# Performance work log

Measured on AMD Instinct MI355X. Metric: run time of the kernel, lower is better.

## Reference

```python
import jax, jax.numpy as jnp
import numpy as np

N_NODES = 50000
N_EDGES = 800000
IN_CH = 128
CH = 128
OUT_CH = 128
N_TAPS = 3
N_LAYERS = 2


def setup_inputs() -> dict:
    key = jax.random.key(0)
    ks = jax.random.split(key, 8)
    s = 0.05
    x = jax.random.normal(ks[0], (N_NODES, IN_CH), dtype=jnp.float32)
    edge_index = jax.random.randint(ks[1], (2, N_EDGES), 0, N_NODES)
    # readin MLP: 1 layer, plain_last=False -> Linear + activation
    w_in = jax.random.normal(ks[2], (IN_CH, CH), dtype=jnp.float32) * s
    b_in = jnp.zeros((CH,), jnp.float32)
    # per-layer GraphFilter taps: (n_taps+1) Linears of [CH, CH]
    taps_w = jax.random.normal(ks[3], (N_LAYERS, N_TAPS + 1, CH, CH), dtype=jnp.float32) * s
    taps_b = jax.random.normal(ks[4], (N_LAYERS, N_TAPS + 1, CH), dtype=jnp.float32) * s
    # readout MLP: 1 layer, plain_last=True -> Linear only
    w_out = jax.random.normal(ks[5], (CH, OUT_CH), dtype=jnp.float32) * s
    b_out = jnp.zeros((OUT_CH,), jnp.float32)
    return {
        "x": x,
        "edge_index": edge_index,
        "w_in": w_in,
        "b_in": b_in,
        "taps_w": taps_w,
        "taps_b": taps_b,
        "w_out": w_out,
        "b_out": b_out,
    }


def reference(x, edge_index, w_in, b_in, taps_w, taps_b, w_out, b_out):
    act = jax.nn.leaky_relu  # torch LeakyReLU default negative_slope=0.01
    src, dst = edge_index[0], edge_index[1]
    n = x.shape[0]

    # readin: Linear + act (plain_last=False)
    h = act(x @ w_in + b_in)

    n_layers, n_taps_p1 = taps_w.shape[0], taps_w.shape[1]
    for l in range(n_layers):
        # ResidualBlock: y = act(h); y = GraphFilter(y); h = h + y
        y = act(h)
        out = y @ taps_w[l, 0] + taps_b[l, 0]
        for k in range(1, n_taps_p1):
            # SimpleConv(aggr='sum'): y_i = sum_{(s->i) in E} y_s
            y = jax.ops.segment_sum(y[src], dst, num_segments=n)
            out = out + y @ taps_w[l, k] + taps_b[l, k]
        h = h + out

    # readout: Linear only (plain_last=True)
    return h @ w_out + b_out
```

## Files before the change

kernel.cpp:

```cpp
#include <hip/hip_runtime.h>

typedef unsigned int uint;
typedef unsigned short ushort;

using bf16x8 = __attribute__((ext_vector_type(8))) short;
using f32x4  = __attribute__((ext_vector_type(4))) float;

__device__ __forceinline__ float lrelu(float v) { return v > 0.f ? v : 0.01f * v; }
__device__ __forceinline__ float b2f(ushort u) { return __uint_as_float((uint)u << 16); }
__device__ __forceinline__ ushort f2b(float f) {
  uint u = __float_as_uint(f);
  u += 0x7fffu + ((u >> 16) & 1u);
  return (ushort)(u >> 16);
}

#define CSR_B 256
#define BKT_SHIFT 10
#define MAX_NB 64


template <int MODE, int K>
__global__ __launch_bounds__(256) void gemm_mfma(
    const ushort* __restrict__ A0, const ushort* __restrict__ A1,
    const ushort* __restrict__ A2, const ushort* __restrict__ A3,
    const ushort* __restrict__ Wt, const float* __restrict__ bias,
    float* __restrict__ h, ushort* __restrict__ yout, int do_act, int N) {
  __shared__ ushort As[64][40];
  __shared__ ushort Bs[128][40];
  const int tid = threadIdx.x;
  const int lane = tid & 63;
  const int wave = tid >> 6;
  const int g = lane >> 4;
  const int mr = lane & 15;
  const int wr = wave >> 1;
  const int wc = wave & 1;
  const int row0 = blockIdx.x * 64;

  const ushort* Ap[4] = {A0, A1, A2, A3};

  f32x4 acc[2][4];
#pragma unroll
  for (int i = 0; i < 2; i++)
#pragma unroll
    for (int j = 0; j < 4; j++) acc[i][j] = (f32x4){0.f, 0.f, 0.f, 0.f};

#pragma unroll 4
  for (int kc = 0; kc < K; kc += 32) {
    {
      int m = tid >> 2, q = tid & 3;
      int r = row0 + m;
      if (r >= N) r = N - 1;
      int kg = kc + q * 8;
      const ushort* ap = Ap[kg >> 7] + ((size_t)((kg >> 5) & 3)) * N * 32 +
                         (size_t)r * 32 + (kg & 31);
      *(uint4*)&As[m][q * 8] = *(const uint4*)ap;
    }
#pragma unroll
    for (int t = 0; t < 2; t++) {
      int slot = tid + t * 256;
      int n = slot >> 2, q = slot & 3;
      *(uint4*)&Bs[n][q * 8] = *(const uint4*)(Wt + (size_t)n * K + kc + q * 8);
    }
    __syncthreads();
    bf16x8 af[2], bf[4];
#pragma unroll
    for (int rt = 0; rt < 2; rt++) af[rt] = *(bf16x8*)&As[wr * 32 + rt * 16 + mr][g * 8];
#pragma unroll
    for (int ct = 0; ct < 4; ct++) bf[ct] = *(bf16x8*)&Bs[wc * 64 + ct * 16 + mr][g * 8];
#pragma unroll
    for (int rt = 0; rt < 2; rt++)
#pragma unroll
      for (int ct = 0; ct < 4; ct++)
        acc[rt][ct] = __builtin_amdgcn_mfma_f32_16x16x32_bf16(af[rt], bf[ct], acc[rt][ct], 0, 0, 0);
    __syncthreads();
  }

#pragma unroll
  for (int rt = 0; rt < 2; rt++) {
#pragma unroll
    for (int i = 0; i < 4; i++) {
      int R = row0 + wr * 32 + rt * 16 + g * 4 + i;
      if (R >= N) continue;
#pragma unroll
      for (int ct = 0; ct < 4; ct++) {
        int c = wc * 64 + ct * 16 + mr;
        float v = acc[rt][ct][i] + bias[c];
        size_t o = (size_t)R * 128 + c;
        size_t oy = (size_t)(c >> 5) * N * 32 + (size_t)R * 32 + (c & 31);
        if (MODE == 0) {
          float hv = lrelu(v);
          h[o] = hv;
          yout[oy] = f2b(lrelu(hv));
        } else if (MODE == 1) {
          float hv = h[o] + v;
          h[o] = hv;
          if (yout) yout[oy] = f2b(do_act ? lrelu(hv) : hv);
        } else {
          h[o] = v;
        }
      }
    }
  }
}

__global__ __launch_bounds__(256) void agg_bf16(const ushort* __restrict__ yin,
                                                ushort* __restrict__ yout,
                                                const int* __restrict__ rowp,
                                                const ushort* __restrict__ esrc, int N) {
  int t = threadIdx.x;
  int chunk = blockIdx.x & 3;
  int node = (blockIdx.x >> 2) * 64 + (t >> 2);
  if (node >= N) return;
  int lane = t & 3;
  const ushort* yb = yin + (size_t)chunk * N * 32 + lane * 8;
  int beg = rowp[node], end = rowp[node + 1];
  float s[8] = {0.f, 0.f, 0.f, 0.f, 0.f, 0.f, 0.f, 0.f};
  int j = beg;
  for (; j + 4 <= end; j += 4) {
    int s0 = esrc[j], s1 = esrc[j + 1], s2 = esrc[j + 2], s3 = esrc[j + 3];
    union { uint4 v; ushort u[8]; } w0, w1, w2, w3;
    w0.v = *(const uint4*)(yb + (size_t)s0 * 32);
    w1.v = *(const uint4*)(yb + (size_t)s1 * 32);
    w2.v = *(const uint4*)(yb + (size_t)s2 * 32);
    w3.v = *(const uint4*)(yb + (size_t)s3 * 32);
#pragma unroll
    for (int e = 0; e < 8; e++)
      s[e] += (b2f(w0.u[e]) + b2f(w1.u[e])) + (b2f(w2.u[e]) + b2f(w3.u[e]));
  }
  for (; j < end; j++) {
    int sn = esrc[j];
    union { uint4 v; ushort u[8]; } w;
    w.v = *(const uint4*)(yb + (size_t)sn * 32);
#pragma unroll
    for (int e = 0; e < 8; e++) s[e] += b2f(w.u[e]);
  }
  union { uint4 v; ushort u[8]; } o;
#pragma unroll
  for (int e = 0; e < 8; e++) o.u[e] = f2b(s[e]);
  *(uint4*)(yout + (size_t)chunk * N * 32 + (size_t)node * 32 + lane * 8) = o.v;
}

__global__ __launch_bounds__(256) void cast_f2b(const float* __restrict__ in,
                                                ushort* __restrict__ out, int N) {
  int i = blockIdx.x * 256 + threadIdx.x;
  if (i >= N * 16) return;
  int node = i >> 4, sub = i & 15;
  float4 a = *(const float4*)(in + (size_t)node * 128 + sub * 8);
  float4 b = *(const float4*)(in + (size_t)node * 128 + sub * 8 + 4);
  float v[8] = {a.x, a.y, a.z, a.w, b.x, b.y, b.z, b.w};
  union { uint4 q; ushort u[8]; } o;
#pragma unroll
  for (int e = 0; e < 8; e++) o.u[e] = f2b(v[e]);
  int chunk = sub >> 2, off = (sub & 3) * 8;
  *(uint4*)(out + (size_t)chunk * N * 32 + (size_t)node * 32 + off) = o.q;
}

__global__ __launch_bounds__(256) void prep_k(const float* __restrict__ w_in,
                                              const float* __restrict__ w_out,
                                              const float* __restrict__ taps_w,
                                              const float* __restrict__ taps_b,
                                              ushort* __restrict__ Wt_in,
                                              ushort* __restrict__ Wt_out,
                                              ushort* __restrict__ Wt_l0,
                                              ushort* __restrict__ Wt_l1,
                                              float* __restrict__ bsum) {
  int gid = blockIdx.x * 256 + threadIdx.x;
  if (gid < 16384) {
    int n = gid >> 7, k = gid & 127;
    Wt_in[gid] = f2b(w_in[k * 128 + n]);
  } else if (gid < 32768) {
    int i = gid - 16384;
    int n = i >> 7, k = i & 127;
    Wt_out[i] = f2b(w_out[k * 128 + n]);
  } else if (gid < 98304) {
    int i = gid - 32768;
    int n = i >> 9, k = i & 511;
    Wt_l0[i] = f2b(taps_w[(size_t)k * 128 + n]);
  } else if (gid < 163840) {
    int i = gid - 98304;
    int n = i >> 9, k = i & 511;
    Wt_l1[i] = f2b(taps_w[(size_t)(512 + k) * 128 + n]);
  } else if (gid < 164096) {
    int i = gid - 163840;
    int l = i >> 7, n = i & 127;
    float s = 0.f;
    for (int k = 0; k < 4; k++) s += taps_b[l * 512 + k * 128 + n];
    bsum[i] = s;
  }
}

__global__ __launch_bounds__(256) void chist_k(const int* __restrict__ dst,
                                               int* __restrict__ H, int E, int NB) {
  __shared__ int hh[MAX_NB];
  if (threadIdx.x < NB) hh[threadIdx.x] = 0;
  __syncthreads();
  int chunk = (E + gridDim.x - 1) / gridDim.x;
  int beg = blockIdx.x * chunk, end = min(E, beg + chunk);
  for (int e = beg + threadIdx.x; e < end; e += 256)
    atomicAdd(&hh[dst[e] >> BKT_SHIFT], 1);
  __syncthreads();
  if (threadIdx.x < NB) H[threadIdx.x * gridDim.x + blockIdx.x] = hh[threadIdx.x];
}

__global__ __launch_bounds__(256) void cscan_k(int* __restrict__ H, int M) {
  __shared__ int sm[256];
  int per = (M + 255) / 256;
  int b0 = threadIdx.x * per;
  int hi = min(M, b0 + per);
  int sum = 0;
  for (int i = b0; i < hi; i++) sum += H[i];
  sm[threadIdx.x] = sum;
  __syncthreads();
  int x = sum;
  for (int off = 1; off < 256; off <<= 1) {
    int tt = (threadIdx.x >= off) ? sm[threadIdx.x - off] : 0;
    __syncthreads();
    x += tt;
    sm[threadIdx.x] = x;
    __syncthreads();
  }
  int run = x - sum;
  for (int i = b0; i < hi; i++) {
    int v = H[i];
    H[i] = run;
    run += v;
  }
}

__global__ __launch_bounds__(256) void cscatter_k(const int* __restrict__ src,
                                                  const int* __restrict__ dst,
                                                  const int* __restrict__ H,
                                                  uint* __restrict__ packed,
                                                  int E, int NB) {
  __shared__ int cur[MAX_NB];
  int chunk = (E + gridDim.x - 1) / gridDim.x;
  int beg = blockIdx.x * chunk, end = min(E, beg + chunk);
  if (threadIdx.x < NB) cur[threadIdx.x] = H[threadIdx.x * gridDim.x + blockIdx.x];
  __syncthreads();
  for (int e = beg + threadIdx.x; e < end; e += 256) {
    int d = dst[e];
    int pos = atomicAdd(&cur[d >> BKT_SHIFT], 1);
    packed[pos] = ((uint)d << 16) | (uint)src[e];
  }
}

__global__ __launch_bounds__(256) void fsort_k(const uint* __restrict__ packed,
                                               const int* __restrict__ H,
                                               ushort* __restrict__ esrc,
                                               int* __restrict__ rowp,
                                               int N, int E, int NB) {
  __shared__ int hist[1 << BKT_SHIFT];
  __shared__ int cur[1 << BKT_SHIFT];
  __shared__ int sm[256];
  const int bkt = blockIdx.x;
  const int base = bkt << BKT_SHIFT;
  const int nb_nodes = min(1 << BKT_SHIFT, N - base);
  const int start = H[bkt * CSR_B];
  const int end = (bkt == NB - 1) ? E : H[(bkt + 1) * CSR_B];

  for (int i = threadIdx.x; i < (1 << BKT_SHIFT); i += 256) hist[i] = 0;
  __syncthreads();
  for (int e = start + threadIdx.x; e < end; e += 256)
    atomicAdd(&hist[(packed[e] >> 16) - base], 1);
  __syncthreads();

  int t4 = threadIdx.x * 4;
  int l0 = hist[t4], l1 = hist[t4 + 1], l2 = hist[t4 + 2], l3 = hist[t4 + 3];
  int ssum = l0 + l1 + l2 + l3;
  sm[threadIdx.x] = ssum;
  __syncthreads();
  int x = ssum;
  for (int off = 1; off < 256; off <<= 1) {
    int tt = (threadIdx.x >= off) ? sm[threadIdx.x - off] : 0;
    __syncthreads();
    x += tt;
    sm[threadIdx.x] = x;
    __syncthreads();
  }
  int c0 = start + x - ssum;
  int c1 = c0 + l0, c2 = c1 + l1, c3 = c2 + l2;
  cur[t4] = c0; cur[t4 + 1] = c1; cur[t4 + 2] = c2; cur[t4 + 3] = c3;
  if (t4 + 0 < nb_nodes) rowp[base + t4 + 0] = c0;
  if (t4 + 1 < nb_nodes) rowp[base + t4 + 1] = c1;
  if (t4 + 2 < nb_nodes) rowp[base + t4 + 2] = c2;
  if (t4 + 3 < nb_nodes) rowp[base + t4 + 3] = c3;
  __syncthreads();

  for (int e = start + threadIdx.x; e < end; e += 256) {
    uint p = packed[e];
    int pos = atomicAdd(&cur[(p >> 16) - base], 1);
    esrc[pos] = (ushort)(p & 0xffffu);
  }
  if (bkt == 0 && threadIdx.x == 0) rowp[N] = E;
}

extern "C" void kernel_launch(void* const* d_in, const int* in_sizes, int n_in,
                              void* d_out, int out_size, void* d_ws, size_t ws_size,
                              hipStream_t stream) {
  const float* x      = (const float*)d_in[0];
  const int*   ei     = (const int*)d_in[1];
  const float* w_in   = (const float*)d_in[2];
  const float* b_in   = (const float*)d_in[3];
  const float* taps_w = (const float*)d_in[4];
  const float* taps_b = (const float*)d_in[5];
  const float* w_out  = (const float*)d_in[6];
  const float* b_out  = (const float*)d_in[7];

  const int N = in_sizes[0] / 128;
  const int E = in_sizes[1] / 2;
  const int* src = ei;
  const int* dst = ei + E;
  const int NB = (N + (1 << BKT_SHIFT) - 1) >> BKT_SHIFT;

  float* h = (float*)d_out;

  const size_t yelem = (size_t)N * 128;
  ushort* y0 = (ushort*)d_ws;
  ushort* y1 = y0 + yelem;
  ushort* y2 = y1 + yelem;
  ushort* y3 = y2 + yelem;
  ushort* Wt_in  = y3 + yelem;
  ushort* Wt_out = Wt_in + 128 * 128;
  ushort* Wt_l0  = Wt_out + 128 * 128;
  ushort* Wt_l1  = Wt_l0 + 128 * 512;
  float*  bsum   = (float*)(Wt_l1 + 128 * 512);
  int*    rowp   = (int*)(bsum + 256);
  int*    H      = rowp + (N + 1);
  uint*   packed = (uint*)(H + MAX_NB * CSR_B);
  ushort* esrc   = (ushort*)(packed + E);

  const int gemmB = (N + 63) / 64;
  const int aggB  = ((N + 63) / 64) * 4;
  const int castB = (N * 16 + 255) / 256;

  chist_k<<<CSR_B, 256, 0, stream>>>(dst, H, E, NB);
  cscan_k<<<1, 256, 0, stream>>>(H, NB * CSR_B);
  cscatter_k<<<CSR_B, 256, 0, stream>>>(src, dst, H, packed, E, NB);
  fsort_k<<<NB, 256, 0, stream>>>(packed, H, esrc, rowp, N, E, NB);

  prep_k<<<641, 256, 0, stream>>>(w_in, w_out, taps_w, taps_b,
                                  Wt_in, Wt_out, Wt_l0, Wt_l1, bsum);
  cast_f2b<<<castB, 256, 0, stream>>>(x, y1, N);

  gemm_mfma<0, 128><<<gemmB, 256, 0, stream>>>(y1, y1, y1, y1, Wt_in, b_in, h, y0, 0, N);

  for (int l = 0; l < 2; l++) {
    const ushort* Wt_l = (l == 0) ? Wt_l0 : Wt_l1;
    agg_bf16<<<aggB, 256, 0, stream>>>(y0, y1, rowp, esrc, N);
    agg_bf16<<<aggB, 256, 0, stream>>>(y1, y2, rowp, esrc, N);
    agg_bf16<<<aggB, 256, 0, stream>>>(y2, y3, rowp, esrc, N);
    gemm_mfma<1, 512><<<gemmB, 256, 0, stream>>>(y0, y1, y2, y3, Wt_l, bsum + l * 128,
                                                 h, y0, (l == 0) ? 1 : 0, N);
  }

  gemm_mfma<2, 128><<<gemmB, 256, 0, stream>>>(y0, y0, y0, y0, Wt_out, b_out,
                                               (float*)d_out, nullptr, 0, N);
}
```

Baseline: 391.8 us.

## Make aggregation persistent with XCC-affine chunk assignment and wider edge unroll

The aggregation kernel becomes a persistent grid of 2048 blocks. Each block reads its XCC id from a hardware register and starts on the feature chunk matching that die. It then pulls 64-node tiles from a per-chunk atomic counter, so each die's L2 mostly holds one 32-channel slice of y. The edge loop now issues 8 gathers per iteration instead of 4 to expose more memory parallelism. This costs an atomic and two block barriers per tile, plus a memset of the counters.

```diff
diff --git a/kernel.cpp b/kernel.cpp
--- a/kernel.cpp
+++ b/kernel.cpp
@@ -12,6 +12,10 @@
   uint u = __float_as_uint(f);
   u += 0x7fffu + ((u >> 16) & 1u);
   return (ushort)(u >> 16);
+}
+
+__device__ __forceinline__ uint get_xcc() {
+  return (uint)__builtin_amdgcn_s_getreg((31 << 11) | 20) & 7u;
 }
 
 #define CSR_B 256
@@ -106,38 +110,59 @@
 __global__ __launch_bounds__(256) void agg_bf16(const ushort* __restrict__ yin,
                                                 ushort* __restrict__ yout,
                                                 const int* __restrict__ rowp,
-                                                const ushort* __restrict__ esrc, int N) {
-  int t = threadIdx.x;
-  int chunk = blockIdx.x & 3;
-  int node = (blockIdx.x >> 2) * 64 + (t >> 2);
-  if (node >= N) return;
-  int lane = t & 3;
-  const ushort* yb = yin + (size_t)chunk * N * 32 + lane * 8;
-  int beg = rowp[node], end = rowp[node + 1];
-  float s[8] = {0.f, 0.f, 0.f, 0.f, 0.f, 0.f, 0.f, 0.f};
-  int j = beg;
-  for (; j + 4 <= end; j += 4) {
-    int s0 = esrc[j], s1 = esrc[j + 1], s2 = esrc[j + 2], s3 = esrc[j + 3];
-    union { uint4 v; ushort u[8]; } w0, w1, w2, w3;
-    w0.v = *(const uint4*)(yb + (size_t)s0 * 32);
-    w1.v = *(const uint4*)(yb + (size_t)s1 * 32);
-    w2.v = *(const uint4*)(yb + (size_t)s2 * 32);
-    w3.v = *(const uint4*)(yb + (size_t)s3 * 32);
-#pragma unroll
-    for (int e = 0; e < 8; e++)
-      s[e] += (b2f(w0.u[e]) + b2f(w1.u[e])) + (b2f(w2.u[e]) + b2f(w3.u[e]));
-  }
-  for (; j < end; j++) {
-    int sn = esrc[j];
-    union { uint4 v; ushort u[8]; } w;
-    w.v = *(const uint4*)(yb + (size_t)sn * 32);
-#pragma unroll
-    for (int e = 0; e < 8; e++) s[e] += b2f(w.u[e]);
-  }
-  union { uint4 v; ushort u[8]; } o;
-#pragma unroll
-  for (int e = 0; e < 8; e++) o.u[e] = f2b(s[e]);
-  *(uint4*)(yout + (size_t)chunk * N * 32 + (size_t)node * 32 + lane * 8) = o.v;
+                                                const ushort* __restrict__ esrc,
+                                                int* __restrict__ cnt, int N) {
+  __shared__ int s_tile;
+  const int T = (N + 63) >> 6;
+  const int t = threadIdx.x;
+  const int lane = t & 3;
+  const int nsub = t >> 2;
+  const uint mychunk = get_xcc() & 3u;
+
+  for (int c = 0; c < 4; c++) {
+    const int chunk = (int)((mychunk + c) & 3u);
+    const ushort* yb = yin + (size_t)chunk * N * 32 + lane * 8;
+    ushort* yo = yout + (size_t)chunk * N * 32 + lane * 8;
+    while (true) {
+      if (t == 0) s_tile = atomicAdd(&cnt[chunk], 1);
+      __syncthreads();
+      const int tile = s_tile;
+      __syncthreads();
+      if (tile >= T) break;
+      const int node = tile * 64 + nsub;
+      if (node < N) {
+        const int beg = rowp[node], end = rowp[node + 1];
+        float s[8] = {0.f, 0.f, 0.f, 0.f, 0.f, 0.f, 0.f, 0.f};
+        int j = beg;
+        for (; j + 8 <= end; j += 8) {
+          union { uint4 v; ushort u[8]; } w[8];
+#pragma unroll
+          for (int u = 0; u < 8; u++) {
+            int sn = esrc[j + u];
+            w[u].v = *(const uint4*)(yb + (size_t)sn * 32);
+          }
+#pragma unroll
+          for (int e = 0; e < 8; e++) {
+            float a = 0.f;
+#pragma unroll
+            for (int u = 0; u < 8; u++) a += b2f(w[u].u[e]);
+            s[e] += a;
+          }
+        }
+        for (; j < end; j++) {
+          int sn = esrc[j];
+          union { uint4 v; ushort u[8]; } w;
+          w.v = *(const uint4*)(yb + (size_t)sn * 32);
+#pragma unroll
+          for (int e = 0; e < 8; e++) s[e] += b2f(w.u[e]);
+        }
+        union { uint4 v; ushort u[8]; } o;
+#pragma unroll
+        for (int e = 0; e < 8; e++) o.u[e] = f2b(s[e]);
+        *(uint4*)(yo + (size_t)node * 32) = o.v;
+      }
+    }
+  }
 }
 
 __global__ __launch_bounds__(256) void cast_f2b(const float* __restrict__ in,
@@ -328,10 +353,13 @@
   int*    H      = rowp + (N + 1);
   uint*   packed = (uint*)(H + MAX_NB * CSR_B);
   ushort* esrc   = (ushort*)(packed + E);
+  int*    cnts   = (int*)(esrc + E + (E & 1));
 
   const int gemmB = (N + 63) / 64;
-  const int aggB  = ((N + 63) / 64) * 4;
   const int castB = (N * 16 + 255) / 256;
+  const int aggB  = 2048;
+
+  hipMemsetAsync(cnts, 0, 24 * sizeof(int), stream);
 
   chist_k<<<CSR_B, 256, 0, stream>>>(dst, H, E, NB);
   cscan_k<<<1, 256, 0, stream>>>(H, NB * CSR_B);
@@ -344,11 +372,12 @@
 
   gemm_mfma<0, 128><<<gemmB, 256, 0, stream>>>(y1, y1, y1, y1, Wt_in, b_in, h, y0, 0, N);
 
+  int agg_i = 0;
   for (int l = 0; l < 2; l++) {
     const ushort* Wt_l = (l == 0) ? Wt_l0 : Wt_l1;
-    agg_bf16<<<aggB, 256, 0, stream>>>(y0, y1, rowp, esrc, N);
-    agg_bf16<<<aggB, 256, 0, stream>>>(y1, y2, rowp, esrc, N);
-    agg_bf16<<<aggB, 256, 0, stream>>>(y2, y3, rowp, esrc, N);
+    agg_bf16<<<aggB, 256, 0, stream>>>(y0, y1, rowp, esrc, cnts + 4 * agg_i++, N);
+    agg_bf16<<<aggB, 256, 0, stream>>>(y1, y2, rowp, esrc, cnts + 4 * agg_i++, N);
+    agg_bf16<<<aggB, 256, 0, stream>>>(y2, y3, rowp, esrc, cnts + 4 * agg_i++, N);
     gemm_mfma<1, 512><<<gemmB, 256, 0, stream>>>(y0, y1, y2, y3, Wt_l, bsum + l * 128,
                                                  h, y0, (l == 0) ? 1 : 0, N);
   }
```

Measured after the change: 1.068 ms. +172.6%, slower.
